# Optimization experiments

Hardware: AMD Instinct MI355X
Metric: run time of the kernel (lower is better)

## Reference

```python
import jax, jax.numpy as jnp
import numpy as np
import math

DX = DZ = DATTN = DOUT = 1024
LX = LZ = 4096

def setup_inputs() -> dict:
    key = jax.random.key(0)
    ks = jax.random.split(key, 6)
    X = jax.random.normal(ks[0], (DX, LX), dtype=jnp.float32)
    Z = jax.random.normal(ks[1], (DZ, LZ), dtype=jnp.float32)
    mask = jax.random.randint(ks[2], (LZ, LX), 0, 2) > 0  # bool (lz, lx)
    Wq = jax.random.normal(ks[3], (DATTN, DX), dtype=jnp.float32) / math.sqrt(DATTN)
    bq = jnp.zeros((DATTN, 1), dtype=jnp.float32)
    Wk = jax.random.normal(ks[4], (DATTN, DZ), dtype=jnp.float32) / math.sqrt(DATTN)
    bk = jnp.zeros((DATTN, 1), dtype=jnp.float32)
    Wv = jax.random.normal(ks[5], (DOUT, DZ), dtype=jnp.float32) / math.sqrt(DOUT)
    bv = jnp.zeros((DOUT, 1), dtype=jnp.float32)
    return {"X": X, "Z": Z, "mask": mask, "Wq": Wq, "bq": bq,
            "Wk": Wk, "bk": bk, "Wv": Wv, "bv": bv}

def reference(X, Z, mask, Wq, bq, Wk, bk, Wv, bv):
    dattn_sqrt = math.sqrt(Wq.shape[0])
    q = Wq @ X + bq                      # (dattn, lx)
    k = Wk @ Z + bk                      # (dattn, lz)
    v = Wv @ Z + bv                      # (dout, lz)
    score = k.T @ q                      # (lz, lx)
    # masked_fill with -1000 happens BEFORE scaling, matching the original
    score = jnp.where(mask, score, jnp.float32(-1000.0))
    attn = jax.nn.softmax(score / dattn_sqrt, axis=0)  # softmax over lz (dim 0)
    return v @ attn                      # (dout, lx)
```

## Files before the change

### kernel.cpp

```cpp
#include <hip/hip_runtime.h>
#include <hip/hip_bf16.h>
#include <math.h>

constexpr int DXc = 1024;
constexpr int DZc = 1024;
constexpr int LXc = 4096;
constexpr int LZc = 4096;
constexpr int DAc = 1024;
constexpr int DOc = 1024;

typedef __attribute__((ext_vector_type(8))) short bf16x8;
typedef __attribute__((ext_vector_type(4))) float f32x4;

__device__ __forceinline__ ushort f2bf(float f) {
    __hip_bfloat16 h = __float2bfloat16(f);
    return *reinterpret_cast<ushort*>(&h);
}
__device__ __forceinline__ float bflo(unsigned u) {
    return __builtin_bit_cast(float, u << 16);
}
__device__ __forceinline__ float bfhi(unsigned u) {
    return __builtin_bit_cast(float, u & 0xffff0000u);
}

enum BiasMode { BIAS_NONE, BIAS_M, BIAS_N };

#define SCHED0() __builtin_amdgcn_sched_barrier(0)
#define BAR2()   do { SCHED0(); __builtin_amdgcn_s_barrier(); SCHED0(); } while (0)
#define LGKM0()  do { asm volatile("s_waitcnt lgkmcnt(0)" ::: "memory"); SCHED0(); } while (0)
#define VMCNT(n) do { asm volatile("s_waitcnt vmcnt(" #n ")" ::: "memory"); SCHED0(); } while (0)

template<BiasMode BMODE, bool OUT_BF16, bool SPLIT>
__device__ __forceinline__ void gemm256(
    const ushort* __restrict__ A, const ushort* __restrict__ B,
    const float* __restrict__ bias, void* __restrict__ Cv,
    int M, int N, int K, int lda, int ldb, int ldc,
    int m0, int n0, int kbase, int zsplit, char* smem)
{
    const int tid  = threadIdx.x;
    const int wid  = tid >> 6, lane = tid & 63;
    const int wr   = wid >> 2, wc = wid & 3;
    const int lrow = lane & 15, quad = lane >> 4;
    const int swz  = (lrow & 7) << 4;
    const int cx0  = (quad * 16) ^ swz;
    const int cx1  = (64 + quad * 16) ^ swz;
    const int raB  = (wr * 16 + lrow) * 128;
    const int rbB  = (wc * 16 + lrow) * 128;

    char* const Ab0 = smem;
    char* const Ab1 = smem + 32768;
    char* const Bb0 = smem + 65536;
    char* const Bb1 = smem + 98304;

    auto stage = [&](const ushort* __restrict__ Mat, int ld, int r0, int kc,
                     char* dstBuf, int h) {
        #pragma unroll
        for (int r = 0; r < 2; ++r) {
            const int q = h * 16384 + r * 8192 + wid * 1024 + lane * 16;
            const int p = q ^ (((q >> 7) & 7) << 4);
            const ushort* g = Mat + (size_t)(r0 + (p >> 7)) * ld + kc + ((p & 127) >> 1);
            __builtin_amdgcn_global_load_lds(
                (const __attribute__((address_space(1))) void*)g,
                (__attribute__((address_space(3))) void*)(dstBuf + h * 16384 + r * 8192 + wid * 1024),
                16, 0, 0);
        }
    };

    f32x4  acc[8][4] = {};
    bf16x8 alo[4][2], ahi[4][2], blo[2][2], bhi[2][2];

    auto ldLo = [&](char* Abuf, char* Bbuf) {
        #pragma unroll
        for (int m = 0; m < 4; ++m) {
            alo[m][0] = *reinterpret_cast<const bf16x8*>(Abuf + m * 4096 + raB + cx0);
            alo[m][1] = *reinterpret_cast<const bf16x8*>(Abuf + m * 4096 + raB + cx1);
        }
        #pragma unroll
        for (int n = 0; n < 2; ++n) {
            blo[n][0] = *reinterpret_cast<const bf16x8*>(Bbuf + n * 8192 + rbB + cx0);
            blo[n][1] = *reinterpret_cast<const bf16x8*>(Bbuf + n * 8192 + rbB + cx1);
        }
    };
    auto ldAhi = [&](char* Abuf) {
        #pragma unroll
        for (int m = 0; m < 4; ++m) {
            ahi[m][0] = *reinterpret_cast<const bf16x8*>(Abuf + (m + 4) * 4096 + raB + cx0);
            ahi[m][1] = *reinterpret_cast<const bf16x8*>(Abuf + (m + 4) * 4096 + raB + cx1);
        }
    };
    auto ldBhi = [&](char* Bbuf) {
        #pragma unroll
        for (int n = 0; n < 2; ++n) {
            bhi[n][0] = *reinterpret_cast<const bf16x8*>(Bbuf + (n + 2) * 8192 + rbB + cx0);
            bhi[n][1] = *reinterpret_cast<const bf16x8*>(Bbuf + (n + 2) * 8192 + rbB + cx1);
        }
    };
    auto mmaQ = [&](bf16x8 (&a)[4][2], bf16x8 (&b)[2][2], int mh, int nh) {
        __builtin_amdgcn_s_setprio(1);
        #pragma unroll
        for (int m = 0; m < 4; ++m)
            #pragma unroll
            for (int n = 0; n < 2; ++n) {
                f32x4& c = acc[mh * 4 + m][nh * 2 + n];
                c = __builtin_amdgcn_mfma_f32_16x16x32_bf16(a[m][0], b[n][0], c, 0, 0, 0);
                c = __builtin_amdgcn_mfma_f32_16x16x32_bf16(a[m][1], b[n][1], c, 0, 0, 0);
            }
        __builtin_amdgcn_s_setprio(0);
    };

    const int NIT = K >> 7;

    stage(A, lda, m0, kbase,      Ab0, 0);
    stage(B, ldb, n0, kbase,      Bb0, 0);
    stage(B, ldb, n0, kbase,      Bb0, 1);
    stage(A, lda, m0, kbase,      Ab0, 1);
    VMCNT(4);
    stage(A, lda, m0, kbase + 64, Ab1, 0);
    stage(B, ldb, n0, kbase + 64, Bb1, 0);
    stage(B, ldb, n0, kbase + 64, Bb1, 1);
    VMCNT(6);
    BAR2();

    #pragma unroll 1
    for (int it = 0; it < NIT; ++it) {
        const bool st  = (it < NIT - 1);
        const int kU   = kbase + (2 * it + 1) * 64;
        const int kT2  = kbase + (2 * it + 2) * 64;
        const int kT3  = kbase + (2 * it + 3) * 64;

        ldLo(Ab0, Bb0);
        stage(A, lda, m0, kU, Ab1, 1);
        asm volatile("s_waitcnt lgkmcnt(8)" ::: "memory");
        BAR2(); LGKM0();
        mmaQ(alo, blo, 0, 0);
        BAR2();
        ldBhi(Bb0);
        if (st) stage(A, lda, m0, kT2, Ab0, 0);
        BAR2(); LGKM0();
        mmaQ(alo, bhi, 0, 1);
        BAR2();
        ldAhi(Ab0);
        if (st) stage(B, ldb, n0, kT2, Bb0, 0);
        BAR2(); LGKM0();
        mmaQ(ahi, bhi, 1, 1);
        BAR2();
        if (st) { stage(B, ldb, n0, kT2, Bb0, 1); VMCNT(6); }
        else    { VMCNT(0); }
        BAR2();
        mmaQ(ahi, blo, 1, 0);
        BAR2();
        ldLo(Ab1, Bb1);
        if (st) stage(A, lda, m0, kT2, Ab0, 1);
        asm volatile("s_waitcnt lgkmcnt(8)" ::: "memory");
        BAR2(); LGKM0();
        mmaQ(alo, blo, 0, 0);
        BAR2();
        ldBhi(Bb1);
        if (st) stage(A, lda, m0, kT3, Ab1, 0);
        BAR2(); LGKM0();
        mmaQ(alo, bhi, 0, 1);
        BAR2();
        ldAhi(Ab1);
        if (st) stage(B, ldb, n0, kT3, Bb1, 0);
        BAR2(); LGKM0();
        mmaQ(ahi, bhi, 1, 1);
        BAR2();
        if (st) { stage(B, ldb, n0, kT3, Bb1, 1); VMCNT(6); }
        else    { VMCNT(0); }
        BAR2();
        mmaQ(ahi, blo, 1, 0);
        BAR2();
    }

    float*  Cf = (float*)Cv + (SPLIT ? (size_t)zsplit * (size_t)M * ldc : 0);
    ushort* Cb = (ushort*)Cv;
    #pragma unroll
    for (int m = 0; m < 8; ++m) {
        const int rowb = m0 + 32 * m + wr * 16 + quad * 4;
        #pragma unroll
        for (int r = 0; r < 4; ++r) {
            const int row = rowb + r;
            const float bm = (BMODE == BIAS_M) ? bias[row] : 0.0f;
            #pragma unroll
            for (int n = 0; n < 4; ++n) {
                const int col = n0 + 64 * n + wc * 16 + lrow;
                float v = acc[m][n][r] + ((BMODE == BIAS_N) ? bias[col] : bm);
                if (OUT_BF16) Cb[(size_t)row * ldc + col] = f2bf(v);
                else          Cf[(size_t)row * ldc + col] = v;
            }
        }
    }
}

__global__ __launch_bounds__(512, 2)
void proj256_kernel(const ushort* __restrict__ XT, const ushort* __restrict__ ZT,
                    const ushort* __restrict__ Wqb, const ushort* __restrict__ Wkb,
                    const ushort* __restrict__ Wvb,
                    const float* __restrict__ bq, const float* __restrict__ bk,
                    const float* __restrict__ bv,
                    ushort* __restrict__ qT, ushort* __restrict__ kT,
                    ushort* __restrict__ vB)
{
    extern __shared__ char smem[];
    int b = blockIdx.x;
    if (b < 64) {
        gemm256<BIAS_N, true, false>(XT, Wqb, bq, qT, LXc, DAc, DXc, DXc, DXc, DAc,
                                     (b >> 2) * 256, (b & 3) * 256, 0, 0, smem);
    } else if (b < 128) {
        b -= 64;
        gemm256<BIAS_N, true, false>(ZT, Wkb, bk, kT, LZc, DAc, DZc, DZc, DZc, DAc,
                                     (b >> 2) * 256, (b & 3) * 256, 0, 0, smem);
    } else {
        b -= 128;
        gemm256<BIAS_M, true, false>(Wvb, ZT, bv, vB, DOc, LZc, DZc, DZc, DZc, LZc,
                                     (b >> 4) * 256, (b & 15) * 256, 0, 0, smem);
    }
}

__global__ __launch_bounds__(512, 2)
void score256_kernel(const ushort* __restrict__ qT, const ushort* __restrict__ kT,
                     ushort* __restrict__ sTb)
{
    extern __shared__ char smem[];
    const int b = blockIdx.x;
    gemm256<BIAS_NONE, true, false>(qT, kT, nullptr, sTb, LXc, LZc, DAc, DAc, DAc, LZc,
                                    (b >> 4) * 256, (b & 15) * 256, 0, 0, smem);
}

__global__ __launch_bounds__(512, 2)
void out256_kernel(const ushort* __restrict__ vB, const ushort* __restrict__ sTb,
                   float* __restrict__ P)
{
    extern __shared__ char smem[];
    gemm256<BIAS_NONE, false, true>(vB, sTb, nullptr, P, DOc, LXc, LZc / 4,
                                    LZc, LZc, LXc,
                                    blockIdx.y * 256, blockIdx.x * 256,
                                    blockIdx.z * (LZc / 4), blockIdx.z, smem);
}

__global__ __launch_bounds__(256)
void prep_kernel(const float* __restrict__ X, const float* __restrict__ Z,
                 const float* __restrict__ Wq, const float* __restrict__ Wk,
                 const float* __restrict__ Wv, const int* __restrict__ mask,
                 ushort* __restrict__ XT, ushort* __restrict__ ZT,
                 ushort* __restrict__ Wqb, ushort* __restrict__ Wkb,
                 ushort* __restrict__ Wvb, unsigned* __restrict__ bits)
{
    __shared__ float tile[32][33];
    const int tid = threadIdx.x;
    int b = blockIdx.x;

    if (b < 8192) {
        const float* in  = (b < 4096) ? X : Z;
        ushort*      out = (b < 4096) ? XT : ZT;
        const int local = b & 4095;
        const int bx = local & 127, by = local >> 7;
        const int c0 = bx * 32, r0 = by * 32;
        const int tx = tid & 31, ty = tid >> 5;
        #pragma unroll
        for (int i = 0; i < 32; i += 8)
            tile[ty + i][tx] = in[(size_t)(r0 + ty + i) * LXc + c0 + tx];
        __syncthreads();
        #pragma unroll
        for (int i = 0; i < 32; i += 8)
            out[(size_t)(c0 + ty + i) * DXc + r0 + tx] = f2bf(tile[tx][ty + i]);
        return;
    }
    if (b < 11264) {
        b -= 8192;
        const float* in  = (b < 1024) ? Wq : (b < 2048) ? Wk : Wv;
        ushort*      out = (b < 1024) ? Wqb : (b < 2048) ? Wkb : Wvb;
        const int local = b & 1023;
        const size_t i = ((size_t)local * 256 + tid) * 4;
        float4 f = *reinterpret_cast<const float4*>(in + i);
        ushort4 u;
        u.x = f2bf(f.x); u.y = f2bf(f.y); u.z = f2bf(f.z); u.w = f2bf(f.w);
        *reinterpret_cast<ushort4*>(out + i) = u;
        return;
    }
    b -= 11264;
    const int xb = b & 15, zb = b >> 4;
    const int x  = xb * 256 + tid;
    const int z0 = zb * 32;
    unsigned w = 0;
    #pragma unroll 8
    for (int i = 0; i < 32; ++i)
        w |= (mask[(size_t)(z0 + i) * LXc + x] != 0 ? 1u : 0u) << i;
    bits[(size_t)x * (LZc / 32) + zb] = w;
}

__global__ __launch_bounds__(256)
void softmax_kernel(ushort* __restrict__ sTb, const unsigned* __restrict__ bits)
{
    const int x   = blockIdx.x;
    const int tid = threadIdx.x;
    ushort* row = sTb + (size_t)x * LZc;
    constexpr float scale = 1.0f / 32.0f;
    constexpr float MASKV = -1000.0f / 32.0f;

    float v[16];
    float mx = -1e30f;
    #pragma unroll
    for (int r = 0; r < 2; ++r) {
        const uint4 pk = *reinterpret_cast<const uint4*>(row + (size_t)(r * 256 + tid) * 8);
        const unsigned* w = reinterpret_cast<const unsigned*>(&pk);
        const unsigned mb = (bits[(size_t)x * 128 + r * 64 + (tid >> 2)] >> ((tid & 3) * 8)) & 0xffu;
        #pragma unroll
        for (int j = 0; j < 4; ++j) {
            const float lo = ((mb >> (2 * j))     & 1u) ? bflo(w[j]) * scale : MASKV;
            const float hi = ((mb >> (2 * j + 1)) & 1u) ? bfhi(w[j]) * scale : MASKV;
            v[r * 8 + 2 * j]     = lo;
            v[r * 8 + 2 * j + 1] = hi;
            mx = fmaxf(mx, fmaxf(lo, hi));
        }
    }
    __shared__ float redmax[4];
    #pragma unroll
    for (int off = 32; off > 0; off >>= 1)
        mx = fmaxf(mx, __shfl_down(mx, off, 64));
    if ((tid & 63) == 0) redmax[tid >> 6] = mx;
    __syncthreads();
    mx = fmaxf(fmaxf(redmax[0], redmax[1]), fmaxf(redmax[2], redmax[3]));

    float sum = 0.0f;
    #pragma unroll
    for (int i = 0; i < 16; ++i) {
        v[i] = __expf(v[i] - mx);
        sum += v[i];
    }
    __shared__ float redsum[4];
    #pragma unroll
    for (int off = 32; off > 0; off >>= 1)
        sum += __shfl_down(sum, off, 64);
    if ((tid & 63) == 0) redsum[tid >> 6] = sum;
    __syncthreads();
    sum = redsum[0] + redsum[1] + redsum[2] + redsum[3];
    const float inv = 1.0f / sum;

    #pragma unroll
    for (int r = 0; r < 2; ++r) {
        uint4 pk;
        unsigned* w = reinterpret_cast<unsigned*>(&pk);
        #pragma unroll
        for (int j = 0; j < 4; ++j) {
            const unsigned lo = f2bf(v[r * 8 + 2 * j] * inv);
            const unsigned hi = f2bf(v[r * 8 + 2 * j + 1] * inv);
            w[j] = lo | (hi << 16);
        }
        *reinterpret_cast<uint4*>(row + (size_t)(r * 256 + tid) * 8) = pk;
    }
}

__global__ __launch_bounds__(256)
void reduce_kernel(const float* __restrict__ P, float* __restrict__ out)
{
    constexpr size_t total = (size_t)DOc * LXc;
    const size_t i = ((size_t)blockIdx.x * 256 + threadIdx.x) * 4;
    float4 s = *reinterpret_cast<const float4*>(P + i);
    #pragma unroll
    for (int p = 1; p < 4; ++p) {
        const float4 t = *reinterpret_cast<const float4*>(P + (size_t)p * total + i);
        s.x += t.x; s.y += t.y; s.z += t.z; s.w += t.w;
    }
    *reinterpret_cast<float4*>(out + i) = s;
}

extern "C" void kernel_launch(void* const* d_in, const int* in_sizes, int n_in,
                              void* d_out, int out_size, void* d_ws, size_t ws_size,
                              hipStream_t stream)
{
    const float* X    = (const float*)d_in[0];
    const float* Z    = (const float*)d_in[1];
    const int*   mask = (const int*)  d_in[2];
    const float* Wq   = (const float*)d_in[3];
    const float* bq   = (const float*)d_in[4];
    const float* Wk   = (const float*)d_in[5];
    const float* bk   = (const float*)d_in[6];
    const float* Wv   = (const float*)d_in[7];
    const float* bv   = (const float*)d_in[8];
    float* out = (float*)d_out;

    static bool inited = false;
    if (!inited) {
        (void)hipFuncSetAttribute((const void*)proj256_kernel,
                                  hipFuncAttributeMaxDynamicSharedMemorySize, 131072);
        (void)hipFuncSetAttribute((const void*)score256_kernel,
                                  hipFuncAttributeMaxDynamicSharedMemorySize, 131072);
        (void)hipFuncSetAttribute((const void*)out256_kernel,
                                  hipFuncAttributeMaxDynamicSharedMemorySize, 131072);
        inited = true;
    }

    char* ws = (char*)d_ws;
    ushort*   XT   = (ushort*)(ws);
    ushort*   ZT   = (ushort*)(ws + ( 8ull << 20));
    ushort*   Wqb  = (ushort*)(ws + (16ull << 20));
    ushort*   Wkb  = (ushort*)(ws + (18ull << 20));
    ushort*   Wvb  = (ushort*)(ws + (20ull << 20));
    ushort*   qT   = (ushort*)(ws + (22ull << 20));
    ushort*   kT   = (ushort*)(ws + (30ull << 20));
    float*    P    = (float*) (ws);
    ushort*   vB   = (ushort*)(ws + (64ull << 20));
    ushort*   sTb  = (ushort*)(ws + (72ull << 20));
    unsigned* bits = (unsigned*)(ws + (104ull << 20));

    prep_kernel<<<dim3(13312), 256, 0, stream>>>(X, Z, Wq, Wk, Wv, mask,
                                                 XT, ZT, Wqb, Wkb, Wvb, bits);
    proj256_kernel<<<dim3(192), 512, 131072, stream>>>(XT, ZT, Wqb, Wkb, Wvb,
                                                       bq, bk, bv, qT, kT, vB);
    score256_kernel<<<dim3(256), 512, 131072, stream>>>(qT, kT, sTb);
    softmax_kernel<<<dim3(LXc), 256, 0, stream>>>(sTb, bits);
    out256_kernel<<<dim3(16, 4, 4), 512, 131072, stream>>>(vB, sTb, P);
    reduce_kernel<<<dim3(DOc * LXc / 1024), 256, 0, stream>>>(P, out);
}
```

Baseline: 280.5 us.

## Move mask bit-packing into projection kernel and store split-K partials in fp16

The mask-to-bits packing moves out of the prep kernel into 64 extra blocks of the projection kernel. These blocks read int4 vectors and fill the idle CUs next to the 192 GEMM blocks. The split-K partial outputs of the final GEMM are written as fp16 instead of fp32, halving partial-buffer write and read traffic, and the reduce kernel handles 8 elements per thread. The cost is fp16 rounding of partial sums, which could overflow or lose precision, and the bits stores are strided and uncoalesced.

```diff
diff --git a/kernel.cpp b/kernel.cpp
--- a/kernel.cpp
+++ b/kernel.cpp
@@ -11,6 +11,7 @@
 
 typedef __attribute__((ext_vector_type(8))) short bf16x8;
 typedef __attribute__((ext_vector_type(4))) float f32x4;
+typedef __attribute__((ext_vector_type(8))) _Float16 f16x8;
 
 __device__ __forceinline__ ushort f2bf(float f) {
     __hip_bfloat16 h = __float2bfloat16(f);
@@ -172,8 +173,8 @@
         BAR2();
     }
 
-    float*  Cf = (float*)Cv + (SPLIT ? (size_t)zsplit * (size_t)M * ldc : 0);
-    ushort* Cb = (ushort*)Cv;
+    _Float16* Ch = (_Float16*)Cv + (SPLIT ? (size_t)zsplit * (size_t)M * ldc : 0);
+    ushort*   Cb = (ushort*)Cv;
     #pragma unroll
     for (int m = 0; m < 8; ++m) {
         const int rowb = m0 + 32 * m + wr * 16 + quad * 4;
@@ -186,7 +187,7 @@
                 const int col = n0 + 64 * n + wc * 16 + lrow;
                 float v = acc[m][n][r] + ((BMODE == BIAS_N) ? bias[col] : bm);
                 if (OUT_BF16) Cb[(size_t)row * ldc + col] = f2bf(v);
-                else          Cf[(size_t)row * ldc + col] = v;
+                else          Ch[(size_t)row * ldc + col] = (_Float16)v;
             }
         }
     }
@@ -199,7 +200,8 @@
                     const float* __restrict__ bq, const float* __restrict__ bk,
                     const float* __restrict__ bv,
                     ushort* __restrict__ qT, ushort* __restrict__ kT,
-                    ushort* __restrict__ vB)
+                    ushort* __restrict__ vB,
+                    const int* __restrict__ mask, unsigned* __restrict__ bits)
 {
     extern __shared__ char smem[];
     int b = blockIdx.x;
@@ -210,10 +212,35 @@
         b -= 64;
         gemm256<BIAS_N, true, false>(ZT, Wkb, bk, kT, LZc, DAc, DZc, DZc, DZc, DAc,
                                      (b >> 2) * 256, (b & 3) * 256, 0, 0, smem);
-    } else {
+    } else if (b < 192) {
         b -= 128;
         gemm256<BIAS_M, true, false>(Wvb, ZT, bv, vB, DOc, LZc, DZc, DZc, DZc, LZc,
                                      (b >> 4) * 256, (b & 15) * 256, 0, 0, smem);
+    } else {
+        const int mb  = b - 192;
+        const int tid = threadIdx.x;
+        #pragma unroll 1
+        for (int zi = 0; zi < 2; ++zi) {
+            const int zb = mb * 2 + zi;
+            #pragma unroll 1
+            for (int rep = 0; rep < 2; ++rep) {
+                const int x = (rep * 512 + tid) * 4;
+                const int* mp = mask + (size_t)(zb * 32) * LXc + x;
+                unsigned w0 = 0, w1 = 0, w2 = 0, w3 = 0;
+                #pragma unroll 8
+                for (int i = 0; i < 32; ++i) {
+                    const int4 m = *reinterpret_cast<const int4*>(mp + (size_t)i * LXc);
+                    w0 |= (m.x != 0 ? 1u : 0u) << i;
+                    w1 |= (m.y != 0 ? 1u : 0u) << i;
+                    w2 |= (m.z != 0 ? 1u : 0u) << i;
+                    w3 |= (m.w != 0 ? 1u : 0u) << i;
+                }
+                bits[(size_t)(x + 0) * (LZc / 32) + zb] = w0;
+                bits[(size_t)(x + 1) * (LZc / 32) + zb] = w1;
+                bits[(size_t)(x + 2) * (LZc / 32) + zb] = w2;
+                bits[(size_t)(x + 3) * (LZc / 32) + zb] = w3;
+            }
+        }
     }
 }
 
@@ -229,7 +256,7 @@
 
 __global__ __launch_bounds__(512, 2)
 void out256_kernel(const ushort* __restrict__ vB, const ushort* __restrict__ sTb,
-                   float* __restrict__ P)
+                   _Float16* __restrict__ P)
 {
     extern __shared__ char smem[];
     gemm256<BIAS_NONE, false, true>(vB, sTb, nullptr, P, DOc, LXc, LZc / 4,
@@ -241,10 +268,10 @@
 __global__ __launch_bounds__(256)
 void prep_kernel(const float* __restrict__ X, const float* __restrict__ Z,
                  const float* __restrict__ Wq, const float* __restrict__ Wk,
-                 const float* __restrict__ Wv, const int* __restrict__ mask,
+                 const float* __restrict__ Wv,
                  ushort* __restrict__ XT, ushort* __restrict__ ZT,
                  ushort* __restrict__ Wqb, ushort* __restrict__ Wkb,
-                 ushort* __restrict__ Wvb, unsigned* __restrict__ bits)
+                 ushort* __restrict__ Wvb)
 {
     __shared__ float tile[32][33];
     const int tid = threadIdx.x;
@@ -266,27 +293,15 @@
             out[(size_t)(c0 + ty + i) * DXc + r0 + tx] = f2bf(tile[tx][ty + i]);
         return;
     }
-    if (b < 11264) {
-        b -= 8192;
-        const float* in  = (b < 1024) ? Wq : (b < 2048) ? Wk : Wv;
-        ushort*      out = (b < 1024) ? Wqb : (b < 2048) ? Wkb : Wvb;
-        const int local = b & 1023;
-        const size_t i = ((size_t)local * 256 + tid) * 4;
-        float4 f = *reinterpret_cast<const float4*>(in + i);
-        ushort4 u;
-        u.x = f2bf(f.x); u.y = f2bf(f.y); u.z = f2bf(f.z); u.w = f2bf(f.w);
-        *reinterpret_cast<ushort4*>(out + i) = u;
-        return;
-    }
-    b -= 11264;
-    const int xb = b & 15, zb = b >> 4;
-    const int x  = xb * 256 + tid;
-    const int z0 = zb * 32;
-    unsigned w = 0;
-    #pragma unroll 8
-    for (int i = 0; i < 32; ++i)
-        w |= (mask[(size_t)(z0 + i) * LXc + x] != 0 ? 1u : 0u) << i;
-    bits[(size_t)x * (LZc / 32) + zb] = w;
+    b -= 8192;
+    const float* in  = (b < 1024) ? Wq : (b < 2048) ? Wk : Wv;
+    ushort*      out = (b < 1024) ? Wqb : (b < 2048) ? Wkb : Wvb;
+    const int local = b & 1023;
+    const size_t i = ((size_t)local * 256 + tid) * 4;
+    float4 f = *reinterpret_cast<const float4*>(in + i);
+    ushort4 u;
+    u.x = f2bf(f.x); u.y = f2bf(f.y); u.z = f2bf(f.z); u.w = f2bf(f.w);
+    *reinterpret_cast<ushort4*>(out + i) = u;
 }
 
 __global__ __launch_bounds__(256)
@@ -352,17 +367,21 @@
 }
 
 __global__ __launch_bounds__(256)
-void reduce_kernel(const float* __restrict__ P, float* __restrict__ out)
+void reduce_kernel(const _Float16* __restrict__ P, float* __restrict__ out)
 {
     constexpr size_t total = (size_t)DOc * LXc;
-    const size_t i = ((size_t)blockIdx.x * 256 + threadIdx.x) * 4;
-    float4 s = *reinterpret_cast<const float4*>(P + i);
-    #pragma unroll
-    for (int p = 1; p < 4; ++p) {
-        const float4 t = *reinterpret_cast<const float4*>(P + (size_t)p * total + i);
-        s.x += t.x; s.y += t.y; s.z += t.z; s.w += t.w;
-    }
-    *reinterpret_cast<float4*>(out + i) = s;
+    const size_t i = ((size_t)blockIdx.x * 256 + threadIdx.x) * 8;
+    float s[8] = {};
+    #pragma unroll
+    for (int p = 0; p < 4; ++p) {
+        const f16x8 t = *reinterpret_cast<const f16x8*>(P + (size_t)p * total + i);
+        #pragma unroll
+        for (int j = 0; j < 8; ++j) s[j] += (float)t[j];
+    }
+    float4 o0 = {s[0], s[1], s[2], s[3]};
+    float4 o1 = {s[4], s[5], s[6], s[7]};
+    *reinterpret_cast<float4*>(out + i)     = o0;
+    *reinterpret_cast<float4*>(out + i + 4) = o1;
 }
 
 extern "C" void kernel_launch(void* const* d_in, const int* in_sizes, int n_in,
@@ -399,17 +418,18 @@
     ushort*   Wvb  = (ushort*)(ws + (20ull << 20));
     ushort*   qT   = (ushort*)(ws + (22ull << 20));
     ushort*   kT   = (ushort*)(ws + (30ull << 20));
-    float*    P    = (float*) (ws);
+    _Float16* P    = (_Float16*)(ws);
     ushort*   vB   = (ushort*)(ws + (64ull << 20));
     ushort*   sTb  = (ushort*)(ws + (72ull << 20));
     unsigned* bits = (unsigned*)(ws + (104ull << 20));
 
-    prep_kernel<<<dim3(13312), 256, 0, stream>>>(X, Z, Wq, Wk, Wv, mask,
-                                                 XT, ZT, Wqb, Wkb, Wvb, bits);
-    proj256_kernel<<<dim3(192), 512, 131072, stream>>>(XT, ZT, Wqb, Wkb, Wvb,
-                                                       bq, bk, bv, qT, kT, vB);
+    prep_kernel<<<dim3(11264), 256, 0, stream>>>(X, Z, Wq, Wk, Wv,
+                                                 XT, ZT, Wqb, Wkb, Wvb);
+    proj256_kernel<<<dim3(256), 512, 131072, stream>>>(XT, ZT, Wqb, Wkb, Wvb,
+                                                       bq, bk, bv, qT, kT, vB,
+                                                       mask, bits);
     score256_kernel<<<dim3(256), 512, 131072, stream>>>(qT, kT, sTb);
     softmax_kernel<<<dim3(LXc), 256, 0, stream>>>(sTb, bits);
     out256_kernel<<<dim3(16, 4, 4), 512, 131072, stream>>>(vB, sTb, P);
-    reduce_kernel<<<dim3(DOc * LXc / 1024), 256, 0, stream>>>(P, out);
-}
+    reduce_kernel<<<dim3(DOc * LXc / 2048), 256, 0, stream>>>(P, out);
+}
```

Result: no change. 280.0 us (-0.2%).

## Fuse softmax, output GEMM and split-K reduction into one kernel with atomic barriers

Applied to the files above, without the earlier changes.

Merges the softmax pass and the split-K partial reduction into the output GEMM kernel. Grid-level dependencies are handled with atomic counters, which are zeroed by an extra block in the prep kernel, and spin-wait barriers. The split-K partials are stored as fp16 instead of fp32, halving their memory traffic. This removes two kernel launches and the separate reduce pass. In exchange it relies on all 256 blocks being co-resident to avoid deadlock, and fp16 partials add precision and overflow risk.

```diff
diff --git a/kernel.cpp b/kernel.cpp
--- a/kernel.cpp
+++ b/kernel.cpp
@@ -11,6 +11,7 @@
 
 typedef __attribute__((ext_vector_type(8))) short bf16x8;
 typedef __attribute__((ext_vector_type(4))) float f32x4;
+typedef __attribute__((ext_vector_type(8))) _Float16 f16x8;
 
 __device__ __forceinline__ ushort f2bf(float f) {
     __hip_bfloat16 h = __float2bfloat16(f);
@@ -172,8 +173,8 @@
         BAR2();
     }
 
-    float*  Cf = (float*)Cv + (SPLIT ? (size_t)zsplit * (size_t)M * ldc : 0);
-    ushort* Cb = (ushort*)Cv;
+    _Float16* Ch = (_Float16*)Cv + (SPLIT ? (size_t)zsplit * (size_t)M * ldc : 0);
+    ushort*   Cb = (ushort*)Cv;
     #pragma unroll
     for (int m = 0; m < 8; ++m) {
         const int rowb = m0 + 32 * m + wr * 16 + quad * 4;
@@ -186,7 +187,7 @@
                 const int col = n0 + 64 * n + wc * 16 + lrow;
                 float v = acc[m][n][r] + ((BMODE == BIAS_N) ? bias[col] : bm);
                 if (OUT_BF16) Cb[(size_t)row * ldc + col] = f2bf(v);
-                else          Cf[(size_t)row * ldc + col] = v;
+                else          Ch[(size_t)row * ldc + col] = (_Float16)v;
             }
         }
     }
@@ -228,14 +229,116 @@
 }
 
 __global__ __launch_bounds__(512, 2)
-void out256_kernel(const ushort* __restrict__ vB, const ushort* __restrict__ sTb,
-                   float* __restrict__ P)
+void outfused_kernel(const ushort* __restrict__ vB, ushort* __restrict__ sTb,
+                     const unsigned* __restrict__ bits, _Float16* __restrict__ P,
+                     float* __restrict__ out, unsigned* __restrict__ cnt)
 {
     extern __shared__ char smem[];
+    const int bx = blockIdx.x, by = blockIdx.y, bz = blockIdx.z;
+    const int lid = bx + 16 * by + 64 * bz;
+    const int tid = threadIdx.x;
+    const int lane = tid & 63, wid = tid >> 6;
+    unsigned* cnt1 = cnt;
+    unsigned* cnt2 = cnt + 16;
+
+    {
+        constexpr float scale = 1.0f / 32.0f;
+        constexpr float MASKV = -1000.0f / 32.0f;
+        #pragma unroll 1
+        for (int i = 0; i < 2; ++i) {
+            const int x = lid * 16 + wid * 2 + i;
+            ushort* row = sTb + (size_t)x * LZc;
+            float v[64];
+            float mx = -1e30f;
+            #pragma unroll
+            for (int r = 0; r < 8; ++r) {
+                const uint4 pk = *reinterpret_cast<const uint4*>(row + (size_t)(r * 512 + lane * 8));
+                const unsigned* wp = reinterpret_cast<const unsigned*>(&pk);
+                const unsigned mb = (bits[(size_t)x * 128 + r * 16 + (lane >> 2)] >> ((lane & 3) * 8)) & 0xffu;
+                #pragma unroll
+                for (int j = 0; j < 4; ++j) {
+                    const float lo = ((mb >> (2 * j))     & 1u) ? bflo(wp[j]) * scale : MASKV;
+                    const float hi = ((mb >> (2 * j + 1)) & 1u) ? bfhi(wp[j]) * scale : MASKV;
+                    v[r * 8 + 2 * j]     = lo;
+                    v[r * 8 + 2 * j + 1] = hi;
+                    mx = fmaxf(mx, fmaxf(lo, hi));
+                }
+            }
+            #pragma unroll
+            for (int off = 32; off > 0; off >>= 1)
+                mx = fmaxf(mx, __shfl_xor(mx, off, 64));
+            float sum = 0.0f;
+            #pragma unroll
+            for (int k = 0; k < 64; ++k) {
+                v[k] = __expf(v[k] - mx);
+                sum += v[k];
+            }
+            #pragma unroll
+            for (int off = 32; off > 0; off >>= 1)
+                sum += __shfl_xor(sum, off, 64);
+            const float inv = 1.0f / sum;
+            #pragma unroll
+            for (int r = 0; r < 8; ++r) {
+                uint4 pk;
+                unsigned* wp = reinterpret_cast<unsigned*>(&pk);
+                #pragma unroll
+                for (int j = 0; j < 4; ++j) {
+                    const unsigned lo = f2bf(v[r * 8 + 2 * j] * inv);
+                    const unsigned hi = f2bf(v[r * 8 + 2 * j + 1] * inv);
+                    wp[j] = lo | (hi << 16);
+                }
+                *reinterpret_cast<uint4*>(row + (size_t)(r * 512 + lane * 8)) = pk;
+            }
+        }
+    }
+    __syncthreads();
+    if (tid == 0) {
+        __builtin_amdgcn_fence(__ATOMIC_RELEASE, "agent");
+        __hip_atomic_fetch_add(&cnt1[lid >> 4], 1u, __ATOMIC_RELAXED, __HIP_MEMORY_SCOPE_AGENT);
+        while (__hip_atomic_load(&cnt1[bx], __ATOMIC_RELAXED, __HIP_MEMORY_SCOPE_AGENT) < 16u)
+            __builtin_amdgcn_s_sleep(2);
+    }
+    __syncthreads();
+    __builtin_amdgcn_fence(__ATOMIC_ACQUIRE, "agent");
+
     gemm256<BIAS_NONE, false, true>(vB, sTb, nullptr, P, DOc, LXc, LZc / 4,
                                     LZc, LZc, LXc,
-                                    blockIdx.y * 256, blockIdx.x * 256,
-                                    blockIdx.z * (LZc / 4), blockIdx.z, smem);
+                                    by * 256, bx * 256, bz * (LZc / 4), bz, smem);
+
+    __syncthreads();
+    if (tid == 0) {
+        __builtin_amdgcn_fence(__ATOMIC_RELEASE, "agent");
+        __hip_atomic_fetch_add(&cnt2[bx + 16 * by], 1u, __ATOMIC_RELAXED, __HIP_MEMORY_SCOPE_AGENT);
+        while (__hip_atomic_load(&cnt2[bx + 16 * by], __ATOMIC_RELAXED, __HIP_MEMORY_SCOPE_AGENT) < 4u)
+            __builtin_amdgcn_s_sleep(2);
+    }
+    __syncthreads();
+    __builtin_amdgcn_fence(__ATOMIC_ACQUIRE, "agent");
+
+    {
+        constexpr size_t total = (size_t)DOc * LXc;
+        const int r  = tid >> 3;
+        const int sg = (tid & 7) * 32;
+        const int o  = by * 256 + bz * 64 + r;
+        const int x0 = bx * 256 + sg;
+        float s[32] = {};
+        #pragma unroll
+        for (int p = 0; p < 4; ++p) {
+            const _Float16* pp = P + (size_t)p * total + (size_t)o * LXc + x0;
+            #pragma unroll
+            for (int v8 = 0; v8 < 4; ++v8) {
+                const f16x8 t = *reinterpret_cast<const f16x8*>(pp + v8 * 8);
+                #pragma unroll
+                for (int j = 0; j < 8; ++j) s[v8 * 8 + j] += (float)t[j];
+            }
+        }
+        float* op = out + (size_t)o * LXc + x0;
+        #pragma unroll
+        for (int q = 0; q < 8; ++q) {
+            float4 o4 = {s[q * 4], s[q * 4 + 1], s[q * 4 + 2], s[q * 4 + 3]};
+            *reinterpret_cast<float4*>(op + q * 4) = o4;
+        }
+    }
 }
 
 __global__ __launch_bounds__(256)
@@ -244,7 +347,8 @@
                  const float* __restrict__ Wv, const int* __restrict__ mask,
                  ushort* __restrict__ XT, ushort* __restrict__ ZT,
                  ushort* __restrict__ Wqb, ushort* __restrict__ Wkb,
-                 ushort* __restrict__ Wvb, unsigned* __restrict__ bits)
+                 ushort* __restrict__ Wvb, unsigned* __restrict__ bits,
+                 unsigned* __restrict__ cnt)
 {
     __shared__ float tile[32][33];
     const int tid = threadIdx.x;
@@ -278,91 +382,19 @@
         *reinterpret_cast<ushort4*>(out + i) = u;
         return;
     }
-    b -= 11264;
-    const int xb = b & 15, zb = b >> 4;
-    const int x  = xb * 256 + tid;
-    const int z0 = zb * 32;
-    unsigned w = 0;
-    #pragma unroll 8
-    for (int i = 0; i < 32; ++i)
-        w |= (mask[(size_t)(z0 + i) * LXc + x] != 0 ? 1u : 0u) << i;
-    bits[(size_t)x * (LZc / 32) + zb] = w;
-}
-
-__global__ __launch_bounds__(256)
-void softmax_kernel(ushort* __restrict__ sTb, const unsigned* __restrict__ bits)
-{
-    const int x   = blockIdx.x;
-    const int tid = threadIdx.x;
-    ushort* row = sTb + (size_t)x * LZc;
-    constexpr float scale = 1.0f / 32.0f;
-    constexpr float MASKV = -1000.0f / 32.0f;
-
-    float v[16];
-    float mx = -1e30f;
-    #pragma unroll
-    for (int r = 0; r < 2; ++r) {
-        const uint4 pk = *reinterpret_cast<const uint4*>(row + (size_t)(r * 256 + tid) * 8);
-        const unsigned* w = reinterpret_cast<const unsigned*>(&pk);
-        const unsigned mb = (bits[(size_t)x * 128 + r * 64 + (tid >> 2)] >> ((tid & 3) * 8)) & 0xffu;
-        #pragma unroll
-        for (int j = 0; j < 4; ++j) {
-            const float lo = ((mb >> (2 * j))     & 1u) ? bflo(w[j]) * scale : MASKV;
-            const float hi = ((mb >> (2 * j + 1)) & 1u) ? bfhi(w[j]) * scale : MASKV;
-            v[r * 8 + 2 * j]     = lo;
-            v[r * 8 + 2 * j + 1] = hi;
-            mx = fmaxf(mx, fmaxf(lo, hi));
-        }
-    }
-    __shared__ float redmax[4];
-    #pragma unroll
-    for (int off = 32; off > 0; off >>= 1)
-        mx = fmaxf(mx, __shfl_down(mx, off, 64));
-    if ((tid & 63) == 0) redmax[tid >> 6] = mx;
-    __syncthreads();
-    mx = fmaxf(fmaxf(redmax[0], redmax[1]), fmaxf(redmax[2], redmax[3]));
-
-    float sum = 0.0f;
-    #pragma unroll
-    for (int i = 0; i < 16; ++i) {
-        v[i] = __expf(v[i] - mx);
-        sum += v[i];
-    }
-    __shared__ float redsum[4];
-    #pragma unroll
-    for (int off = 32; off > 0; off >>= 1)
-        sum += __shfl_down(sum, off, 64);
-    if ((tid & 63) == 0) redsum[tid >> 6] = sum;
-    __syncthreads();
-    sum = redsum[0] + redsum[1] + redsum[2] + redsum[3];
-    const float inv = 1.0f / sum;
-
-    #pragma unroll
-    for (int r = 0; r < 2; ++r) {
-        uint4 pk;
-        unsigned* w = reinterpret_cast<unsigned*>(&pk);
-        #pragma unroll
-        for (int j = 0; j < 4; ++j) {
-            const unsigned lo = f2bf(v[r * 8 + 2 * j] * inv);
-            const unsigned hi = f2bf(v[r * 8 + 2 * j + 1] * inv);
-            w[j] = lo | (hi << 16);
-        }
-        *reinterpret_cast<uint4*>(row + (size_t)(r * 256 + tid) * 8) = pk;
-    }
-}
-
-__global__ __launch_bounds__(256)
-void reduce_kernel(const float* __restrict__ P, float* __restrict__ out)
-{
-    constexpr size_t total = (size_t)DOc * LXc;
-    const size_t i = ((size_t)blockIdx.x * 256 + threadIdx.x) * 4;
-    float4 s = *reinterpret_cast<const float4*>(P + i);
-    #pragma unroll
-    for (int p = 1; p < 4; ++p) {
-        const float4 t = *reinterpret_cast<const float4*>(P + (size_t)p * total + i);
-        s.x += t.x; s.y += t.y; s.z += t.z; s.w += t.w;
-    }
-    *reinterpret_cast<float4*>(out + i) = s;
+    if (b < 13312) {
+        b -= 11264;
+        const int xb = b & 15, zb = b >> 4;
+        const int x  = xb * 256 + tid;
+        const int z0 = zb * 32;
+        unsigned w = 0;
+        #pragma unroll 8
+        for (int i = 0; i < 32; ++i)
+            w |= (mask[(size_t)(z0 + i) * LXc + x] != 0 ? 1u : 0u) << i;
+        bits[(size_t)x * (LZc / 32) + zb] = w;
+        return;
+    }
+    if (tid < 80) cnt[tid] = 0u;
 }
 
 extern "C" void kernel_launch(void* const* d_in, const int* in_sizes, int n_in,
@@ -386,7 +418,7 @@
                                   hipFuncAttributeMaxDynamicSharedMemorySize, 131072);
         (void)hipFuncSetAttribute((const void*)score256_kernel,
                                   hipFuncAttributeMaxDynamicSharedMemorySize, 131072);
-        (void)hipFuncSetAttribute((const void*)out256_kernel,
+        (void)hipFuncSetAttribute((const void*)outfused_kernel,
                                   hipFuncAttributeMaxDynamicSharedMemorySize, 131072);
         inited = true;
     }
@@ -399,17 +431,16 @@
     ushort*   Wvb  = (ushort*)(ws + (20ull << 20));
     ushort*   qT   = (ushort*)(ws + (22ull << 20));
     ushort*   kT   = (ushort*)(ws + (30ull << 20));
-    float*    P    = (float*) (ws);
+    _Float16* P    = (_Float16*)(ws);
+    unsigned* cnt  = (unsigned*)(ws + (60ull << 20));
     ushort*   vB   = (ushort*)(ws + (64ull << 20));
     ushort*   sTb  = (ushort*)(ws + (72ull << 20));
     unsigned* bits = (unsigned*)(ws + (104ull << 20));
 
-    prep_kernel<<<dim3(13312), 256, 0, stream>>>(X, Z, Wq, Wk, Wv, mask,
-                                                 XT, ZT, Wqb, Wkb, Wvb, bits);
+    prep_kernel<<<dim3(13313), 256, 0, stream>>>(X, Z, Wq, Wk, Wv, mask,
+                                                 XT, ZT, Wqb, Wkb, Wvb, bits, cnt);
     proj256_kernel<<<dim3(192), 512, 131072, stream>>>(XT, ZT, Wqb, Wkb, Wvb,
                                                        bq, bk, bv, qT, kT, vB);
     score256_kernel<<<dim3(256), 512, 131072, stream>>>(qT, kT, sTb);
-    softmax_kernel<<<dim3(LXc), 256, 0, stream>>>(sTb, bits);
-    out256_kernel<<<dim3(16, 4, 4), 512, 131072, stream>>>(vB, sTb, P);
-    reduce_kernel<<<dim3(DOc * LXc / 1024), 256, 0, stream>>>(P, out);
-}
+    outfused_kernel<<<dim3(16, 4, 4), 512, 131072, stream>>>(vB, sTb, bits, P, out, cnt);
+}
```

After: 331.0 us. +18.0%, slower.
